# Kernel optimization log

Measured on AMD Instinct MI355X. Metric: run time of the kernel, lower is better.

Reference implementation:

```python
import jax, jax.numpy as jnp
import numpy as np

K = 1024
H = 16
B = 2
T = 2048


def setup_inputs() -> dict:
    key = jax.random.key(0)
    ks = jax.random.split(key, 8)
    x = jax.random.normal(ks[0], (B, T, K), dtype=jnp.float32)
    mask = jax.random.randint(ks[1], (B, T), 0, 2, dtype=jnp.int32)
    scale = 1.0 / np.sqrt(K)
    Wk = jax.random.normal(ks[2], (K, K), dtype=jnp.float32) * scale
    Wq = jax.random.normal(ks[3], (K, K), dtype=jnp.float32) * scale
    Wv = jax.random.normal(ks[4], (K, K), dtype=jnp.float32) * scale
    Wu = jax.random.normal(ks[5], (K, K), dtype=jnp.float32) * scale
    bu = jnp.zeros((K,), dtype=jnp.float32)
    return {"x": x, "mask": mask, "Wk": Wk, "Wq": Wq, "Wv": Wv, "Wu": Wu, "bu": bu}


def reference(x, mask, Wk, Wq, Wv, Wu, bu):
    b, t, k = x.shape
    h = H
    s = k // h
    # Linear(k, k, bias=False): y = x @ W.T
    keys = (x @ Wk.T).reshape(b, t, h, s)
    queries = (x @ Wq.T).reshape(b, t, h, s)
    values = (x @ Wv.T).reshape(b, t, h, s)
    # raw scores [b, h, t, t]; NOTE: original applies NO 1/sqrt(s) scaling
    raw = jnp.einsum("bqhd,bkhd->bhqk", queries, keys)
    # mask [b, t] broadcast over heads and query positions (keys masked)
    raw = jnp.where(mask[:, None, None, :] == 0, -jnp.inf, raw)
    weights = jax.nn.softmax(raw, axis=-1)
    ys = jnp.einsum("bhqk,bkhd->bqhd", weights, values).reshape(b, t, k)
    return ys @ Wu.T + bu
```

## Files before the change

kernel.cpp:

```cpp
#include <hip/hip_runtime.h>
#include <hip/hip_bf16.h>
#include <math.h>

#define TS 2048
#define KD 1024
#define NH 16
#define SD 64
#define MB 4096
#define LOG2E 1.4426950408889634f

typedef __attribute__((ext_vector_type(8))) short bf16x8;
typedef __attribute__((ext_vector_type(4))) short bf16x4;
typedef __attribute__((ext_vector_type(4))) float f32x4;
typedef unsigned short ushort_t;

#define MFMA32(a, b, c) __builtin_amdgcn_mfma_f32_16x16x32_bf16(a, b, c, 0, 0, 0)

union frag8 { bf16x8 v8; bf16x4 h[2]; };

__device__ __forceinline__ ushort_t f2bf_rn(float f) {
    union { __hip_bfloat16 h; ushort_t u; } c;
    c.h = __float2bfloat16(f);
    return c.u;
}
__device__ __forceinline__ float bf2f(ushort_t u) {
    union { unsigned u; float f; } v; v.u = ((unsigned)u) << 16;
    return v.f;
}
__device__ __forceinline__ ushort4 pk4_bf(float a, float b, float c, float d) {
    union { __hip_bfloat162 h; ushort2 u; } x, y;
    x.h = __float22bfloat162_rn(make_float2(a, b));
    y.h = __float22bfloat162_rn(make_float2(c, d));
    return make_ushort4(x.u.x, x.u.y, y.u.x, y.u.y);
}
__device__ __forceinline__ void gload_lds16(const void* g, void* l) {
    __builtin_amdgcn_global_load_lds(
        (const __attribute__((address_space(1))) unsigned int*)g,
        (__attribute__((address_space(3))) unsigned int*)l, 16, 0, 0);
}

__global__ __launch_bounds__(256)
void conv_all(const float* __restrict__ x, const float* __restrict__ wq,
              const float* __restrict__ wk, const float* __restrict__ wv,
              const float* __restrict__ wu,
              ushort_t* XH, ushort_t* XL, ushort_t* WqH, ushort_t* WqL,
              ushort_t* WkH, ushort_t* WkL, ushort_t* WvH, ushort_t* WuH)
{
    int z = blockIdx.y;
    const float* src; ushort_t* H; ushort_t* L = nullptr; int nblk;
    switch (z) {
        case 0:  src = x;  H = XH;  L = XL;  nblk = 4096; break;
        case 1:  src = wq; H = WqH; L = WqL; nblk = 1024; break;
        case 2:  src = wk; H = WkH; L = WkL; nblk = 1024; break;
        case 3:  src = wv; H = WvH;          nblk = 1024; break;
        default: src = wu; H = WuH;          nblk = 1024; break;
    }
    if ((int)blockIdx.x >= nblk) return;
    int idx = blockIdx.x * 256 + threadIdx.x;
    float4 v = ((const float4*)src)[idx];
    if (z == 1) { v.x *= LOG2E; v.y *= LOG2E; v.z *= LOG2E; v.w *= LOG2E; }
    ushort_t h0 = f2bf_rn(v.x), h1 = f2bf_rn(v.y);
    ushort_t h2 = f2bf_rn(v.z), h3 = f2bf_rn(v.w);
    ((ushort4*)H)[idx] = make_ushort4(h0, h1, h2, h3);
    if (L) {
        ushort_t l0 = f2bf_rn(v.x - bf2f(h0)), l1 = f2bf_rn(v.y - bf2f(h1));
        ushort_t l2 = f2bf_rn(v.z - bf2f(h2)), l3 = f2bf_rn(v.w - bf2f(h3));
        ((ushort4*)L)[idx] = make_ushort4(l0, l1, l2, l3);
    }
}

__global__ __launch_bounds__(256)
void gemm_bf16(const ushort_t* __restrict__ Ah, const ushort_t* __restrict__ Al,
               const ushort_t* __restrict__ Bqh, const ushort_t* __restrict__ Bql,
               const ushort_t* __restrict__ Bkh, const ushort_t* __restrict__ Bkl,
               const ushort_t* __restrict__ Bvh, const ushort_t* __restrict__ Buh,
               ushort_t* __restrict__ OQh, ushort_t* __restrict__ OQl,
               ushort_t* __restrict__ OKh, ushort_t* __restrict__ OKl,
               ushort_t* __restrict__ OVt, float* __restrict__ OF,
               const float* __restrict__ bias, int epi_base)
{
    const int epi = epi_base + blockIdx.z;
    const ushort_t* Bh; const ushort_t* Bl = nullptr;
    if      (epi == 0) { Bh = Bqh; Bl = Bql; }
    else if (epi == 1) { Bh = Bkh; Bl = Bkl; }
    else if (epi == 2) { Bh = Bvh; }
    else               { Bh = Buh; }
    const bool terms3 = (epi < 2);

    __shared__ ushort_t sAh[64 * 32];
    __shared__ ushort_t sAl[64 * 32];
    __shared__ ushort_t sBh[128 * 32];
    __shared__ ushort_t sBl[128 * 32];

    const int tid = threadIdx.x;
    const int wave = tid >> 6, lane = tid & 63;
    const int col = lane & 15, quad = lane >> 4;
    const int wm = wave >> 1, wn = wave & 1;
    const int m0 = blockIdx.y * 64, n0 = blockIdx.x * 128;

    f32x4 acc[2][4];
#pragma unroll
    for (int i = 0; i < 2; ++i)
#pragma unroll
        for (int j = 0; j < 4; ++j) acc[i][j] = (f32x4){0.f, 0.f, 0.f, 0.f};

    for (int k0 = 0; k0 < KD; k0 += 32) {
        {
            int row = tid >> 2, k8 = tid & 3;
            int lo  = wave * 64 * 8;
            gload_lds16(Ah + (size_t)(m0 + row) * KD + k0 + k8 * 8, sAh + lo);
            if (terms3)
                gload_lds16(Al + (size_t)(m0 + row) * KD + k0 + k8 * 8, sAl + lo);
        }
#pragma unroll
        for (int j = 0; j < 2; ++j) {
            int s   = wave * 128 + j * 64 + lane;
            int row = s >> 2, k8 = s & 3;
            int lo  = (wave * 128 + j * 64) * 8;
            gload_lds16(Bh + (size_t)(n0 + row) * KD + k0 + k8 * 8, sBh + lo);
            if (terms3)
                gload_lds16(Bl + (size_t)(n0 + row) * KD + k0 + k8 * 8, sBl + lo);
        }
        __syncthreads();

        bf16x8 fbh[4], fbl[4];
#pragma unroll
        for (int j = 0; j < 4; ++j) {
            int r = (wn * 64 + j * 16 + col) * 32 + quad * 8;
            fbh[j] = *(const bf16x8*)&sBh[r];
            if (terms3) fbl[j] = *(const bf16x8*)&sBl[r];
        }
#pragma unroll
        for (int i = 0; i < 2; ++i) {
            int r = (wm * 32 + i * 16 + col) * 32 + quad * 8;
            bf16x8 fah = *(const bf16x8*)&sAh[r];
            if (terms3) {
                bf16x8 fal = *(const bf16x8*)&sAl[r];
#pragma unroll
                for (int j = 0; j < 4; ++j) {
                    acc[i][j] = MFMA32(fah, fbh[j], acc[i][j]);
                    acc[i][j] = MFMA32(fah, fbl[j], acc[i][j]);
                    acc[i][j] = MFMA32(fal, fbh[j], acc[i][j]);
                }
            } else {
#pragma unroll
                for (int j = 0; j < 4; ++j)
                    acc[i][j] = MFMA32(fah, fbh[j], acc[i][j]);
            }
        }
        __syncthreads();
    }

    if (epi <= 1) {
        ushort_t* OH = (epi == 0) ? OQh : OKh;
        ushort_t* OL = (epi == 0) ? OQl : OKl;
#pragma unroll
        for (int i = 0; i < 2; ++i) {
            int m = m0 + wm * 32 + i * 16 + quad * 4;
#pragma unroll
            for (int j = 0; j < 4; ++j) {
                int n = n0 + wn * 64 + j * 16 + col;
#pragma unroll
                for (int r = 0; r < 4; ++r) {
                    float v = acc[i][j][r];
                    ushort_t hv = f2bf_rn(v);
                    size_t off = (size_t)(m + r) * KD + n;
                    OH[off] = hv;
                    OL[off] = f2bf_rn(v - bf2f(hv));
                }
            }
        }
    } else if (epi == 2) {
#pragma unroll
        for (int i = 0; i < 2; ++i) {
            int m = m0 + wm * 32 + i * 16 + quad * 4;
            int bb = m >> 11, t = m & (TS - 1);
#pragma unroll
            for (int j = 0; j < 4; ++j) {
                int n = n0 + wn * 64 + j * 16 + col;
                int hh = n >> 6, d = n & 63;
                ushort4 pk = pk4_bf(acc[i][j][0], acc[i][j][1], acc[i][j][2], acc[i][j][3]);
                *(ushort4*)(OVt + ((size_t)(bb * NH + hh) * SD + d) * TS + t) = pk;
            }
        }
    } else {
#pragma unroll
        for (int i = 0; i < 2; ++i) {
            int m = m0 + wm * 32 + i * 16 + quad * 4;
#pragma unroll
            for (int j = 0; j < 4; ++j) {
                int n = n0 + wn * 64 + j * 16 + col;
                float bj = bias[n];
#pragma unroll
                for (int r = 0; r < 4; ++r)
                    OF[(size_t)(m + r) * KD + n] = acc[i][j][r] + bj;
            }
        }
    }
}

__global__ __launch_bounds__(256, 2)
void attn_mfma(const ushort_t* __restrict__ QH, const ushort_t* __restrict__ QL,
               const ushort_t* __restrict__ KH, const ushort_t* __restrict__ KL,
               const ushort_t* __restrict__ VT, const int* __restrict__ mask,
               ushort_t* __restrict__ YH)
{
    const int bh = blockIdx.x;
    const int qt = blockIdx.y;
    const int h  = bh & (NH - 1);
    const int b  = bh >> 4;

    const int tid  = threadIdx.x;
    const int wave = tid >> 6;
    const int lane = tid & 63;
    const int col  = lane & 15;
    const int quad = lane >> 4;

    __shared__ ushort_t smem[12288];
    ushort_t* sKH = smem;
    ushort_t* sKL = smem + 4096;
    ushort_t* sVT = smem + 8192;
    __shared__ float lred[4][64];

    bf16x8 bqh[4][2], bql[4][2];
#pragma unroll
    for (int qf = 0; qf < 4; ++qf) {
        size_t qrow = (size_t)(b * TS + qt * 64 + qf * 16 + col) * KD + h * SD;
#pragma unroll
        for (int c = 0; c < 2; ++c) {
            bqh[qf][c] = *(const bf16x8*)(QH + qrow + c * 32 + quad * 8);
            bql[qf][c] = *(const bf16x8*)(QL + qrow + c * 32 + quad * 8);
        }
    }

    const int l8 = lane >> 3, l7 = lane & 7;
    const ushort_t* gp[6];
    ushort_t* ld[6];
#pragma unroll
    for (int r = 0; r < 6; ++r) {
        int cc  = (r & 1) * 4 + wave;
        int row = cc * 8 + l8;
        int gs  = l7 ^ (row & 7);
        if (r < 2)      gp[r] = KH + (size_t)(b * TS + row) * KD + h * SD + gs * 8;
        else if (r < 4) gp[r] = KL + (size_t)(b * TS + row) * KD + h * SD + gs * 8;
        else            gp[r] = VT + ((size_t)bh * SD + row) * TS + gs * 8;
        ld[r] = ((r < 2) ? sKH : (r < 4) ? sKL : sVT) + cc * 512;
    }
    const int* mp = mask + b * TS + wave * 16 + quad * 4;

    float lp[4] = {0.f, 0.f, 0.f, 0.f};
    f32x4 O[4][4];
#pragma unroll
    for (int dt = 0; dt < 4; ++dt)
#pragma unroll
        for (int qf = 0; qf < 4; ++qf) O[dt][qf] = (f32x4){0.f, 0.f, 0.f, 0.f};

    frag8 av[4], bp4[4];
#pragma unroll
    for (int i = 0; i < 4; ++i) {
        av[i].v8  = (bf16x8){0, 0, 0, 0, 0, 0, 0, 0};
        bp4[i].v8 = (bf16x8){0, 0, 0, 0, 0, 0, 0, 0};
    }

    for (int kt = 0; kt < TS / 64; ++kt) {
#pragma unroll
        for (int r = 0; r < 6; ++r) gload_lds16(gp[r], ld[r]);
        int4 mv = *(const int4*)mp;
        mp += 64;
#pragma unroll
        for (int r = 0; r < 6; ++r) gp[r] += (r < 4) ? 64 * KD : 64;
        __syncthreads();

        f32x4 sinit;
        sinit[0] = mv.x ? 0.f : -INFINITY;
        sinit[1] = mv.y ? 0.f : -INFINITY;
        sinit[2] = mv.z ? 0.f : -INFINITY;
        sinit[3] = mv.w ? 0.f : -INFINITY;

        bf16x8 akh[2], akl[2];
#pragma unroll
        for (int c = 0; c < 2; ++c) {
            int sl = (c * 4 + quad) ^ (col & 7);
            akh[c] = *(const bf16x8*)&sKH[((wave * 16 + col) * 8 + sl) * 8];
            akl[c] = *(const bf16x8*)&sKL[((wave * 16 + col) * 8 + sl) * 8];
        }
#pragma unroll
        for (int dt = 0; dt < 4; ++dt) {
            int sl = (wave * 2 + (quad >> 1)) ^ (col & 7);
            av[dt].h[0] = *(const bf16x4*)&sVT[((dt * 16 + col) * 8 + sl) * 8 + (quad & 1) * 4];
        }

#pragma unroll
        for (int qf = 0; qf < 4; ++qf) {
            f32x4 s1 = sinit;
            f32x4 s2 = (f32x4){0.f, 0.f, 0.f, 0.f};
            s1 = MFMA32(akh[0], bqh[qf][0], s1);
            s2 = MFMA32(akl[0], bqh[qf][0], s2);
            s2 = MFMA32(akh[0], bql[qf][0], s2);
            s1 = MFMA32(akh[1], bqh[qf][1], s1);
            s2 = MFMA32(akl[1], bqh[qf][1], s2);
            s2 = MFMA32(akh[1], bql[qf][1], s2);
            float p0 = exp2f(s1[0] + s2[0]);
            float p1 = exp2f(s1[1] + s2[1]);
            float p2 = exp2f(s1[2] + s2[2]);
            float p3 = exp2f(s1[3] + s2[3]);
            lp[qf] += (p0 + p1) + (p2 + p3);
            union { ushort4 u4; bf16x4 v4; } pk;
            pk.u4 = pk4_bf(p0, p1, p2, p3);
            bp4[qf].h[0] = pk.v4;
        }

#pragma unroll
        for (int dt = 0; dt < 4; ++dt)
#pragma unroll
            for (int qf = 0; qf < 4; ++qf)
                O[dt][qf] = MFMA32(av[dt].v8, bp4[qf].v8, O[dt][qf]);

        __syncthreads();
    }

#pragma unroll
    for (int qf = 0; qf < 4; ++qf) {
        float v = lp[qf];
        v += __shfl_xor(v, 16);
        v += __shfl_xor(v, 32);
        if (lane < 16) lred[wave][qf * 16 + lane] = v;
    }

    float* Of = (float*)smem;
#pragma unroll
    for (int w = 1; w < 4; ++w) {
        __syncthreads();
        if (wave == w) {
#pragma unroll
            for (int dt = 0; dt < 4; ++dt)
#pragma unroll
                for (int qf = 0; qf < 4; ++qf)
                    *(f32x4*)&Of[((dt * 4 + qf) * 64 + lane) * 4] = O[dt][qf];
        }
        __syncthreads();
        if (wave == 0) {
#pragma unroll
            for (int dt = 0; dt < 4; ++dt)
#pragma unroll
                for (int qf = 0; qf < 4; ++qf)
                    O[dt][qf] += *(const f32x4*)&Of[((dt * 4 + qf) * 64 + lane) * 4];
        }
    }
    if (wave == 0) {
        float linv[4];
#pragma unroll
        for (int qf = 0; qf < 4; ++qf) {
            int q = qf * 16 + col;
            linv[qf] = 1.f / (lred[0][q] + lred[1][q] + lred[2][q] + lred[3][q]);
        }
#pragma unroll
        for (int dt = 0; dt < 4; ++dt)
#pragma unroll
            for (int qf = 0; qf < 4; ++qf) {
                ushort4 pk = pk4_bf(O[dt][qf][0] * linv[qf], O[dt][qf][1] * linv[qf],
                                    O[dt][qf][2] * linv[qf], O[dt][qf][3] * linv[qf]);
                *(ushort4*)(YH + (size_t)(b * TS + qt * 64 + qf * 16 + col) * KD +
                            h * SD + dt * 16 + quad * 4) = pk;
            }
    }
}

extern "C" void kernel_launch(void* const* d_in, const int* in_sizes, int n_in,
                              void* d_out, int out_size, void* d_ws, size_t ws_size,
                              hipStream_t stream) {
    const float* x    = (const float*)d_in[0];
    const int*   mask = (const int*)d_in[1];
    const float* Wk   = (const float*)d_in[2];
    const float* Wq   = (const float*)d_in[3];
    const float* Wv   = (const float*)d_in[4];
    const float* Wu   = (const float*)d_in[5];
    const float* bu   = (const float*)d_in[6];
    float* out = (float*)d_out;

    char* w = (char*)d_ws;
    const size_t M1 = (size_t)1 << 20;
    ushort_t* XH  = (ushort_t*)(w);
    ushort_t* XL  = (ushort_t*)(w + 8  * M1);
    ushort_t* WqH = (ushort_t*)(w + 16 * M1);
    ushort_t* WqL = (ushort_t*)(w + 18 * M1);
    ushort_t* WkH = (ushort_t*)(w + 20 * M1);
    ushort_t* WkL = (ushort_t*)(w + 22 * M1);
    ushort_t* WvH = (ushort_t*)(w + 24 * M1);
    ushort_t* QHb = (ushort_t*)(w + 26 * M1);
    ushort_t* QLb = (ushort_t*)(w + 34 * M1);
    ushort_t* KHb = (ushort_t*)(w + 42 * M1);
    ushort_t* KLb = (ushort_t*)(w + 50 * M1);
    ushort_t* WuH = (ushort_t*)(w + 58 * M1);
    ushort_t* VTb = (ushort_t*)d_out;
    ushort_t* YHb = (ushort_t*)(w);

    dim3 blk(256);
    conv_all<<<dim3(4096, 5), blk, 0, stream>>>(x, Wq, Wk, Wv, Wu,
                                                XH, XL, WqH, WqL, WkH, WkL, WvH, WuH);
    gemm_bf16<<<dim3(8, 64, 3), blk, 0, stream>>>(XH, XL, WqH, WqL, WkH, WkL, WvH, WuH,
                                                  QHb, QLb, KHb, KLb, VTb, nullptr,
                                                  nullptr, 0);
    attn_mfma<<<dim3(NH * 2, 32), blk, 0, stream>>>(QHb, QLb, KHb, KLb, VTb, mask, YHb);
    gemm_bf16<<<dim3(8, 64, 1), blk, 0, stream>>>(YHb, nullptr, WqH, WqL, WkH, WkL, WvH, WuH,
                                                  nullptr, nullptr, nullptr, nullptr, nullptr,
                                                  out, bu, 3);
}
```

Before: 300.1 us.

## Double-buffer K/V tiles in attention kernel to overlap loads with MFMA

Splits the attention kernel's shared-memory staging into two buffers so the async global-to-LDS load of the next K/V tile is issued before computing on the current one. This removes one barrier per iteration and hides load latency behind the score and PV MFMAs. Launch bounds also rise from 2 to 3 blocks per CU, which tightens the register budget. LDS use doubles to about 48KB per block, which may itself limit occupancy and could cause register spills.

```diff
diff --git a/kernel.cpp b/kernel.cpp
--- a/kernel.cpp
+++ b/kernel.cpp
@@ -199,7 +199,7 @@
     }
 }
 
-__global__ __launch_bounds__(256, 2)
+__global__ __launch_bounds__(256, 3)
 void attn_mfma(const ushort_t* __restrict__ QH, const ushort_t* __restrict__ QL,
                const ushort_t* __restrict__ KH, const ushort_t* __restrict__ KL,
                const ushort_t* __restrict__ VT, const int* __restrict__ mask,
@@ -216,10 +216,7 @@
     const int col  = lane & 15;
     const int quad = lane >> 4;
 
-    __shared__ ushort_t smem[12288];
-    ushort_t* sKH = smem;
-    ushort_t* sKL = smem + 4096;
-    ushort_t* sVT = smem + 8192;
+    __shared__ ushort_t smem[2][12288];
     __shared__ float lred[4][64];
 
     bf16x8 bqh[4][2], bql[4][2];
@@ -235,7 +232,7 @@
 
     const int l8 = lane >> 3, l7 = lane & 7;
     const ushort_t* gp[6];
-    ushort_t* ld[6];
+    int ldoff[6];
 #pragma unroll
     for (int r = 0; r < 6; ++r) {
         int cc  = (r & 1) * 4 + wave;
@@ -244,9 +241,18 @@
         if (r < 2)      gp[r] = KH + (size_t)(b * TS + row) * KD + h * SD + gs * 8;
         else if (r < 4) gp[r] = KL + (size_t)(b * TS + row) * KD + h * SD + gs * 8;
         else            gp[r] = VT + ((size_t)bh * SD + row) * TS + gs * 8;
-        ld[r] = ((r < 2) ? sKH : (r < 4) ? sKL : sVT) + cc * 512;
+        ldoff[r] = ((r < 2) ? 0 : (r < 4) ? 4096 : 8192) + cc * 512;
     }
     const int* mp = mask + b * TS + wave * 16 + quad * 4;
+
+#define STAGE(bsel)                                                         \
+    do {                                                                    \
+        _Pragma("unroll")                                                   \
+        for (int r = 0; r < 6; ++r) {                                       \
+            gload_lds16(gp[r], &smem[bsel][ldoff[r]]);                      \
+            gp[r] += (r < 4) ? 64 * KD : 64;                                \
+        }                                                                   \
+    } while (0)
 
     float lp[4] = {0.f, 0.f, 0.f, 0.f};
     f32x4 O[4][4];
@@ -255,6 +261,7 @@
 #pragma unroll
         for (int qf = 0; qf < 4; ++qf) O[dt][qf] = (f32x4){0.f, 0.f, 0.f, 0.f};
 
+    bf16x8 akh[2], akl[2];
     frag8 av[4], bp4[4];
 #pragma unroll
     for (int i = 0; i < 4; ++i) {
@@ -262,34 +269,29 @@
         bp4[i].v8 = (bf16x8){0, 0, 0, 0, 0, 0, 0, 0};
     }
 
-    for (int kt = 0; kt < TS / 64; ++kt) {
-#pragma unroll
-        for (int r = 0; r < 6; ++r) gload_lds16(gp[r], ld[r]);
-        int4 mv = *(const int4*)mp;
-        mp += 64;
-#pragma unroll
-        for (int r = 0; r < 6; ++r) gp[r] += (r < 4) ? 64 * KD : 64;
-        __syncthreads();
-
+    auto loadfrags = [&](int bsel) {
+        const ushort_t* sKH = smem[bsel];
+        const ushort_t* sKL = smem[bsel] + 4096;
+        const ushort_t* sVT = smem[bsel] + 8192;
+#pragma unroll
+        for (int c = 0; c < 2; ++c) {
+            int sl = (c * 4 + quad) ^ (col & 7);
+            akh[c] = *(const bf16x8*)&sKH[((wave * 16 + col) * 8 + sl) * 8];
+            akl[c] = *(const bf16x8*)&sKL[((wave * 16 + col) * 8 + sl) * 8];
+        }
+#pragma unroll
+        for (int dt = 0; dt < 4; ++dt) {
+            int sl = (wave * 2 + (quad >> 1)) ^ (col & 7);
+            av[dt].h[0] = *(const bf16x4*)&sVT[((dt * 16 + col) * 8 + sl) * 8 + (quad & 1) * 4];
+        }
+    };
+
+    auto domath = [&](int4 mv) {
         f32x4 sinit;
         sinit[0] = mv.x ? 0.f : -INFINITY;
         sinit[1] = mv.y ? 0.f : -INFINITY;
         sinit[2] = mv.z ? 0.f : -INFINITY;
         sinit[3] = mv.w ? 0.f : -INFINITY;
-
-        bf16x8 akh[2], akl[2];
-#pragma unroll
-        for (int c = 0; c < 2; ++c) {
-            int sl = (c * 4 + quad) ^ (col & 7);
-            akh[c] = *(const bf16x8*)&sKH[((wave * 16 + col) * 8 + sl) * 8];
-            akl[c] = *(const bf16x8*)&sKL[((wave * 16 + col) * 8 + sl) * 8];
-        }
-#pragma unroll
-        for (int dt = 0; dt < 4; ++dt) {
-            int sl = (wave * 2 + (quad >> 1)) ^ (col & 7);
-            av[dt].h[0] = *(const bf16x4*)&sVT[((dt * 16 + col) * 8 + sl) * 8 + (quad & 1) * 4];
-        }
-
 #pragma unroll
         for (int qf = 0; qf < 4; ++qf) {
             f32x4 s1 = sinit;
@@ -309,14 +311,28 @@
             pk.u4 = pk4_bf(p0, p1, p2, p3);
             bp4[qf].h[0] = pk.v4;
         }
-
 #pragma unroll
         for (int dt = 0; dt < 4; ++dt)
 #pragma unroll
             for (int qf = 0; qf < 4; ++qf)
                 O[dt][qf] = MFMA32(av[dt].v8, bp4[qf].v8, O[dt][qf]);
-
-        __syncthreads();
+    };
+
+    STAGE(0);
+    int4 mv_cur = *(const int4*)mp; mp += 64;
+    int4 mv_nxt = mv_cur;
+    for (int kt = 0; kt < TS / 64; kt += 2) {
+        __syncthreads();
+        loadfrags(0);
+        if (kt + 1 < TS / 64) { STAGE(1); mv_nxt = *(const int4*)mp; mp += 64; }
+        domath(mv_cur);
+        mv_cur = mv_nxt;
+
+        __syncthreads();
+        loadfrags(1);
+        if (kt + 2 < TS / 64) { STAGE(0); mv_nxt = *(const int4*)mp; mp += 64; }
+        domath(mv_cur);
+        mv_cur = mv_nxt;
     }
 
 #pragma unroll
@@ -327,7 +343,7 @@
         if (lane < 16) lred[wave][qf * 16 + lane] = v;
     }
 
-    float* Of = (float*)smem;
+    float* Of = (float*)&smem[0][0];
 #pragma unroll
     for (int w = 1; w < 4; ++w) {
         __syncthreads();
@@ -364,6 +380,7 @@
                             h * SD + dt * 16 + quad * 4) = pk;
             }
     }
+#undef STAGE
 }
 
 extern "C" void kernel_launch(void* const* d_in, const int* in_sizes, int n_in,
```

Result: slower. 864.1 us (+187.9%).
